# Optimization experiments

Hardware: AMD Instinct MI355X
Metric: run time of the kernel (lower is better)

Reference implementation:

```python
import jax, jax.numpy as jnp
import numpy as np
import math

TWO_PI = 2.0 * math.pi
LN_EPS = 1e-5


def _phase(pos_f, d):
    # periods[i, j] = i * d + j + 2 ; phi[s, i, j] = cos(2*pi*k_s / periods[i, j])
    i = jnp.arange(d, dtype=jnp.float32)
    periods = i[:, None] * d + i[None, :] + 2.0  # (d, d)
    return jnp.cos(TWO_PI * pos_f[:, None, None] / periods)  # (S, d, d)


def _layernorm(x, g, b):
    mu = jnp.mean(x, axis=-1, keepdims=True)
    var = jnp.mean(jnp.square(x - mu), axis=-1, keepdims=True)
    return (x - mu) * jax.lax.rsqrt(var + LN_EPS) * g + b


def _pos_nk(x, P, phi):
    # Nk[b, s, i] = sum_j P[i, j] * x[b, s, j] * phi[s, i, j]
    return jnp.einsum('bsj,ij,sij->bsi', x, P, phi)


def setup_inputs() -> dict:
    key = jax.random.key(0)
    ks = jax.random.split(key, 10)
    B, S, V, D = 4, 4096, 64, 128
    NTOK = 64  # 4^3 k-mer tokens
    u = lambda k, shp, a: jax.random.uniform(k, shp, jnp.float32, -a, a)
    return {
        'tokens': jax.random.randint(ks[0], (B, S), 0, NTOK, dtype=jnp.int32),
        'positions': jnp.arange(S, dtype=jnp.int32),
        'emb': jax.random.normal(ks[1], (NTOK, V), jnp.float32),
        'char_P': u(ks[2], (V, V), 0.1),
        'M1': u(ks[3], (D, V), 0.5),
        'P1': u(ks[4], (D, D), 0.1),
        'g1': jnp.ones((D,), jnp.float32),
        'b1': jnp.zeros((D,), jnp.float32),
        'R1': u(ks[5], (D, V), 0.1),
        'M2': u(ks[6], (D, D), 0.5),
        'P2': u(ks[7], (D, D), 0.1),
        'g2': jnp.ones((D,), jnp.float32),
        'b2': jnp.zeros((D,), jnp.float32),
    }


def reference(tokens, positions, emb, char_P, M1, P1, g1, b1, R1, M2, P2, g2, b2):
    pos_f = positions.astype(jnp.float32)
    V, D1, D2 = emb.shape[1], M1.shape[0], M2.shape[0]
    # char level (Layer 0): embedding + position-modulated mixing
    x = emb[tokens]                               # (B, S, V)
    h = _pos_nk(x, char_P, _phase(pos_f, V))      # (B, S, V)
    # Layer 1: separate residual (in_dim != out_dim -> linear proj)
    t1 = jnp.einsum('bsj,ij->bsi', h, M1)         # (B, S, D1)
    n1 = _pos_nk(_layernorm(t1, g1, b1), P1, _phase(pos_f, D1))
    h1 = n1 + jnp.einsum('bsj,ij->bsi', h, R1)
    # Layer 2: shared residual (residual = x @ M.T, pre-norm)
    t2 = jnp.einsum('bsj,ij->bsi', h1, M2)        # (B, S, D2)
    n2 = _pos_nk(_layernorm(t2, g2, b2), P2, _phase(pos_f, D2))
    return n2 + t2
```

## Files before the change

kernel.cpp:

```cpp
#include <hip/hip_runtime.h>

typedef unsigned short u16;
typedef unsigned int   u32;

#define BB 4
#define SS 4096
#define VV 64
#define DD 128

#define CPT_OFF 0
#define M1T_OFF 4096
#define R1T_OFF 12288
#define P1T_OFF 20480
#define M2T_OFF 36864
#define P2T_OFF 53248
#define EMB_OFF 69632
#define G1_OFF  73728
#define B1_OFF  73856
#define G2_OFF  73984
#define B2_OFF  74112
#define WS_F32_NEEDED 74240

__device__ __forceinline__ float bf2f(u16 u) {
    return __uint_as_float(((u32)u) << 16);
}
__device__ __forceinline__ float ldany(const void* p, int idx, bool f32) {
    return f32 ? ((const float*)p)[idx] : bf2f(((const u16*)p)[idx]);
}
__device__ __forceinline__ float phase_cos(float pos, float pf) {
    float x = pos * __builtin_amdgcn_rcpf(pf);
    float r = x - floorf(x);
    return __builtin_amdgcn_cosf(r);
}

__global__ void prep_ws(const void* __restrict__ cP,  const void* __restrict__ M1,
                        const void* __restrict__ R1,  const void* __restrict__ P1,
                        const void* __restrict__ M2,  const void* __restrict__ P2,
                        const void* __restrict__ emb, const void* __restrict__ g1,
                        const void* __restrict__ b1,  const void* __restrict__ g2,
                        const void* __restrict__ b2,  float* __restrict__ wsf)
{
    const bool f32 = (((const u32*)g1)[0] == 0x3F800000u);
    const int m = blockIdx.x;
    const int t = threadIdx.x;
    if (m == 6) {
        for (int idx = t; idx < 4608; idx += 256) {
            float v; int dst;
            if (idx < 4096) { v = ldany(emb, idx, f32); dst = EMB_OFF + idx; }
            else {
                int off = idx - 4096, which = off >> 7, e = off & 127;
                const void* p = (which == 0) ? g1 : (which == 1) ? b1
                              : (which == 2) ? g2 : b2;
                v = ldany(p, e, f32);
                dst = G1_OFF + which * 128 + e;
            }
            wsf[dst] = v;
        }
        return;
    }
    __shared__ float tile[64][65];
    const void* src; float* dst; int R, C;
    switch (m) {
        case 0:  src = cP; dst = wsf + CPT_OFF; R = 64;  C = 64;  break;
        case 1:  src = M1; dst = wsf + M1T_OFF; R = 128; C = 64;  break;
        case 2:  src = R1; dst = wsf + R1T_OFF; R = 128; C = 64;  break;
        case 3:  src = P1; dst = wsf + P1T_OFF; R = 128; C = 128; break;
        case 4:  src = M2; dst = wsf + M2T_OFF; R = 128; C = 128; break;
        default: src = P2; dst = wsf + P2T_OFF; R = 128; C = 128; break;
    }
    for (int ti0 = 0; ti0 < R; ti0 += 64) {
        for (int tj0 = 0; tj0 < C; tj0 += 64) {
            __syncthreads();
            #pragma unroll
            for (int k = 0; k < 16; ++k) {
                int idx = k * 256 + t;
                int i = idx >> 6, j = idx & 63;
                tile[i][j] = ldany(src, (ti0 + i) * C + (tj0 + j), f32);
            }
            __syncthreads();
            #pragma unroll
            for (int k = 0; k < 16; ++k) {
                int idx = k * 256 + t;
                int j = idx >> 6, i = idx & 63;
                int gj = tj0 + j, gi = ti0 + i;
                dst[((gj >> 2) * R + gi) * 4 + (gj & 3)] = tile[i][j];
            }
        }
    }
}

template<bool WS>
__global__ void __launch_bounds__(256, 4)
fused_hier(const int* __restrict__ tokens,
           const int* __restrict__ positions,
           const void* __restrict__ emb,
           const void* __restrict__ cP,
           const void* __restrict__ M1,
           const void* __restrict__ P1,
           const void* __restrict__ g1,
           const void* __restrict__ b1,
           const void* __restrict__ R1,
           const void* __restrict__ M2,
           const void* __restrict__ P2,
           const void* __restrict__ g2,
           const void* __restrict__ b2,
           const float* __restrict__ wsf,
           float* __restrict__ out)
{
    __shared__ float4 x4v[VV];
    __shared__ float4 h4v[VV];
    __shared__ float4 lnv[DD];
    __shared__ float4 h1v[DD];
    __shared__ float4 t2v[DD];
    __shared__ float4 partv[512];
    __shared__ float  t14[DD * BB];

    float* lnf  = (float*)lnv;
    float* h1f  = (float*)h1v;
    float* t2f  = (float*)t2v;
    float* part = (float*)partv;
    float* h4   = (float*)h4v;
    float* x4   = (float*)x4v;

    const int t = threadIdx.x;
    const int s = blockIdx.x;
    if (s >= SS) return;
    const bool f32 = WS ? true : (((const u32*)g1)[0] == 0x3F800000u);
    const float pos = (float)positions[s];
    const int i6 = t & 63,  q4 = t >> 6;
    const int i7 = t & 127, h2 = t >> 7;
    const int w  = t >> 6,  l  = t & 63;

    {
        int tok = tokens[q4 * SS + s];
        float v = WS ? wsf[EMB_OFF + tok * VV + i6] : ldany(emb, tok * VV + i6, f32);
        x4[i6 * 4 + q4] = v;
    }
    __syncthreads();

    {
        float a0 = 0.f, a1 = 0.f, a2 = 0.f, a3 = 0.f;
        const int jb = q4 * 16;
        float pf = (float)(i6 * VV + jb + 2);
        #pragma unroll
        for (int q = 0; q < 4; ++q) {
            const int jg = q4 * 4 + q;
            float4 w4;
            if (WS) w4 = *(const float4*)&wsf[CPT_OFF + (jg * VV + i6) * 4];
            #pragma unroll
            for (int k = 0; k < 4; ++k) {
                const int j = jb + q * 4 + k;
                float c  = phase_cos(pos, pf);
                float wt = (WS ? ((const float*)&w4)[k]
                               : ldany(cP, i6 * VV + j, f32)) * c;
                float4 xb = x4v[j];
                a0 = fmaf(wt, xb.x, a0); a1 = fmaf(wt, xb.y, a1);
                a2 = fmaf(wt, xb.z, a2); a3 = fmaf(wt, xb.w, a3);
                pf += 1.0f;
            }
        }
        partv[i6 * 4 + q4] = make_float4(a0, a1, a2, a3);
    }
    __syncthreads();

    {
        const int b = q4, i = i6;
        h4[i * 4 + b] = part[(i * 4 + 0) * 4 + b] + part[(i * 4 + 1) * 4 + b]
                      + part[(i * 4 + 2) * 4 + b] + part[(i * 4 + 3) * 4 + b];
    }
    __syncthreads();

    {
        float4 at = make_float4(0, 0, 0, 0), ar = make_float4(0, 0, 0, 0);
        #pragma unroll
        for (int q = 0; q < 8; ++q) {
            const int jg = h2 * 8 + q;
            float4 m4, r4;
            if (WS) {
                m4 = *(const float4*)&wsf[M1T_OFF + (jg * DD + i7) * 4];
                r4 = *(const float4*)&wsf[R1T_OFF + (jg * DD + i7) * 4];
            }
            #pragma unroll
            for (int k = 0; k < 4; ++k) {
                const int j = h2 * 32 + q * 4 + k;
                float mv = WS ? ((const float*)&m4)[k] : ldany(M1, i7 * VV + j, f32);
                float rv = WS ? ((const float*)&r4)[k] : ldany(R1, i7 * VV + j, f32);
                float4 hb = h4v[j];
                at.x = fmaf(mv, hb.x, at.x); at.y = fmaf(mv, hb.y, at.y);
                at.z = fmaf(mv, hb.z, at.z); at.w = fmaf(mv, hb.w, at.w);
                ar.x = fmaf(rv, hb.x, ar.x); ar.y = fmaf(rv, hb.y, ar.y);
                ar.z = fmaf(rv, hb.z, ar.z); ar.w = fmaf(rv, hb.w, ar.w);
            }
        }
        partv[i7 * 2 + h2]       = at;
        partv[256 + i7 * 2 + h2] = ar;
    }
    __syncthreads();

    {
        #pragma unroll
        for (int k = 0; k < 2; ++k) {
            const int b = h2 * 2 + k;
            t14[i7 * 4 + b] = part[(i7 * 2 + 0) * 4 + b] + part[(i7 * 2 + 1) * 4 + b];
            h1f[i7 * 4 + b] = part[1024 + (i7 * 2 + 0) * 4 + b]
                            + part[1024 + (i7 * 2 + 1) * 4 + b];
        }
    }
    __syncthreads();

    {
        float v0 = t14[l * 4 + w], v1 = t14[(l + 64) * 4 + w];
        float s1 = v0 + v1;
        #pragma unroll
        for (int m = 1; m < 64; m <<= 1) s1 += __shfl_xor(s1, m, 64);
        float mu = s1 * (1.0f / 128.0f);
        float d0 = v0 - mu, d1 = v1 - mu;
        float s2 = d0 * d0 + d1 * d1;
        #pragma unroll
        for (int m = 1; m < 64; m <<= 1) s2 += __shfl_xor(s2, m, 64);
        float rs = rsqrtf(s2 * (1.0f / 128.0f) + 1e-5f);
        float ga = WS ? wsf[G1_OFF + l]      : ldany(g1, l, f32);
        float gb = WS ? wsf[G1_OFF + l + 64] : ldany(g1, l + 64, f32);
        float ba = WS ? wsf[B1_OFF + l]      : ldany(b1, l, f32);
        float bb = WS ? wsf[B1_OFF + l + 64] : ldany(b1, l + 64, f32);
        lnf[l * 4 + w]        = d0 * rs * ga + ba;
        lnf[(l + 64) * 4 + w] = d1 * rs * gb + bb;
    }
    __syncthreads();

    {
        float4 acc = make_float4(0, 0, 0, 0);
        float pf = (float)(i7 * DD + h2 * 64 + 2);
        #pragma unroll
        for (int q = 0; q < 16; ++q) {
            const int jg = h2 * 16 + q;
            float4 w4;
            if (WS) w4 = *(const float4*)&wsf[P1T_OFF + (jg * DD + i7) * 4];
            #pragma unroll
            for (int k = 0; k < 4; ++k) {
                const int j = h2 * 64 + q * 4 + k;
                float c = phase_cos(pos, pf);
                float wt = (WS ? ((const float*)&w4)[k]
                               : ldany(P1, i7 * DD + j, f32)) * c;
                float4 lb = lnv[j];
                acc.x = fmaf(wt, lb.x, acc.x); acc.y = fmaf(wt, lb.y, acc.y);
                acc.z = fmaf(wt, lb.z, acc.z); acc.w = fmaf(wt, lb.w, acc.w);
                pf += 1.0f;
            }
        }
        partv[i7 * 2 + h2] = acc;
    }
    __syncthreads();

    {
        #pragma unroll
        for (int k = 0; k < 2; ++k) {
            const int b = h2 * 2 + k;
            h1f[i7 * 4 + b] += part[(i7 * 2 + 0) * 4 + b] + part[(i7 * 2 + 1) * 4 + b];
        }
    }
    __syncthreads();

    {
        float4 acc = make_float4(0, 0, 0, 0);
        #pragma unroll
        for (int q = 0; q < 16; ++q) {
            const int jg = h2 * 16 + q;
            float4 m4;
            if (WS) m4 = *(const float4*)&wsf[M2T_OFF + (jg * DD + i7) * 4];
            #pragma unroll
            for (int k = 0; k < 4; ++k) {
                const int j = h2 * 64 + q * 4 + k;
                float mv = WS ? ((const float*)&m4)[k] : ldany(M2, i7 * DD + j, f32);
                float4 hb = h1v[j];
                acc.x = fmaf(mv, hb.x, acc.x); acc.y = fmaf(mv, hb.y, acc.y);
                acc.z = fmaf(mv, hb.z, acc.z); acc.w = fmaf(mv, hb.w, acc.w);
            }
        }
        partv[i7 * 2 + h2] = acc;
    }
    __syncthreads();

    {
        #pragma unroll
        for (int k = 0; k < 2; ++k) {
            const int b = h2 * 2 + k;
            t2f[i7 * 4 + b] = part[(i7 * 2 + 0) * 4 + b] + part[(i7 * 2 + 1) * 4 + b];
        }
    }
    __syncthreads();

    {
        float v0 = t2f[l * 4 + w], v1 = t2f[(l + 64) * 4 + w];
        float s1 = v0 + v1;
        #pragma unroll
        for (int m = 1; m < 64; m <<= 1) s1 += __shfl_xor(s1, m, 64);
        float mu = s1 * (1.0f / 128.0f);
        float d0 = v0 - mu, d1 = v1 - mu;
        float s2 = d0 * d0 + d1 * d1;
        #pragma unroll
        for (int m = 1; m < 64; m <<= 1) s2 += __shfl_xor(s2, m, 64);
        float rs = rsqrtf(s2 * (1.0f / 128.0f) + 1e-5f);
        float ga = WS ? wsf[G2_OFF + l]      : ldany(g2, l, f32);
        float gb = WS ? wsf[G2_OFF + l + 64] : ldany(g2, l + 64, f32);
        float ba = WS ? wsf[B2_OFF + l]      : ldany(b2, l, f32);
        float bb = WS ? wsf[B2_OFF + l + 64] : ldany(b2, l + 64, f32);
        lnf[l * 4 + w]        = d0 * rs * ga + ba;
        lnf[(l + 64) * 4 + w] = d1 * rs * gb + bb;
    }
    __syncthreads();

    {
        float4 acc = make_float4(0, 0, 0, 0);
        float pf = (float)(i7 * DD + h2 * 64 + 2);
        #pragma unroll
        for (int q = 0; q < 16; ++q) {
            const int jg = h2 * 16 + q;
            float4 w4;
            if (WS) w4 = *(const float4*)&wsf[P2T_OFF + (jg * DD + i7) * 4];
            #pragma unroll
            for (int k = 0; k < 4; ++k) {
                const int j = h2 * 64 + q * 4 + k;
                float c = phase_cos(pos, pf);
                float wt = (WS ? ((const float*)&w4)[k]
                               : ldany(P2, i7 * DD + j, f32)) * c;
                float4 lb = lnv[j];
                acc.x = fmaf(wt, lb.x, acc.x); acc.y = fmaf(wt, lb.y, acc.y);
                acc.z = fmaf(wt, lb.z, acc.z); acc.w = fmaf(wt, lb.w, acc.w);
                pf += 1.0f;
            }
        }
        partv[i7 * 2 + h2] = acc;
    }
    __syncthreads();

    {
        #pragma unroll
        for (int k = 0; k < 2; ++k) {
            const int b = h2 * 2 + k;
            float v = part[(i7 * 2 + 0) * 4 + b] + part[(i7 * 2 + 1) * 4 + b]
                    + t2f[i7 * 4 + b];
            out[(b * SS + s) * DD + i7] = v;
        }
    }
}

extern "C" void kernel_launch(void* const* d_in, const int* in_sizes, int n_in,
                              void* d_out, int out_size, void* d_ws, size_t ws_size,
                              hipStream_t stream)
{
    const int* tokens    = (const int*)d_in[0];
    const int* positions = (const int*)d_in[1];
    const void* emb = d_in[2];
    const void* cP  = d_in[3];
    const void* M1  = d_in[4];
    const void* P1  = d_in[5];
    const void* g1  = d_in[6];
    const void* b1  = d_in[7];
    const void* R1  = d_in[8];
    const void* M2  = d_in[9];
    const void* P2  = d_in[10];
    const void* g2  = d_in[11];
    const void* b2  = d_in[12];
    float* out = (float*)d_out;
    float* wsf = (float*)d_ws;

    const bool tw = (ws_size >= (size_t)WS_F32_NEEDED * sizeof(float));
    if (tw) {
        prep_ws<<<7, 256, 0, stream>>>(cP, M1, R1, P1, M2, P2, emb, g1, b1, g2, b2, wsf);
        fused_hier<true><<<SS, 256, 0, stream>>>(tokens, positions, emb, cP, M1, P1,
                                                 g1, b1, R1, M2, P2, g2, b2, wsf, out);
    } else {
        fused_hier<false><<<SS, 256, 0, stream>>>(tokens, positions, emb, cP, M1, P1,
                                                  g1, b1, R1, M2, P2, g2, b2, wsf, out);
    }
}
```

Before: 168.8 us.

## Precompute bf16 phase-cosine table in workspace and reuse across layers

Adds a prep pass with one block per position that writes a bf16 table of the 128x128 phase cosines into workspace. The fused kernel loads these instead of evaluating rcp/floor/cos per element, and one table serves both the char layer (a 64x64 subset via period indexing) and both 128-wide layers. It also moves partial-sum buffers to a float4 batch-packed layout and simplifies reductions and output stores. The cost is about 128 MB of table writes and reads per call, plus bf16 rounding of the phase values.

```diff
diff --git a/kernel.cpp b/kernel.cpp
--- a/kernel.cpp
+++ b/kernel.cpp
@@ -19,7 +19,10 @@
 #define B1_OFF  73856
 #define G2_OFF  73984
 #define B2_OFF  74112
-#define WS_F32_NEEDED 74240
+#define WS_F32_WEIGHTS 74240
+#define PH_BYTE      ((size_t)WS_F32_WEIGHTS * 4)
+#define PH_ROW_BYTES 32768
+#define WS_BYTES_TABLE (PH_BYTE + (size_t)SS * (size_t)PH_ROW_BYTES)
 
 __device__ __forceinline__ float bf2f(u16 u) {
     return __uint_as_float(((u32)u) << 16);
@@ -31,6 +34,27 @@
     float x = pos * __builtin_amdgcn_rcpf(pf);
     float r = x - floorf(x);
     return __builtin_amdgcn_cosf(r);
+}
+__device__ __forceinline__ u32 f2bf(float f) {
+    u32 b = __float_as_uint(f);
+    b += 0x7FFFu + ((b >> 16) & 1u);
+    return b >> 16;
+}
+__device__ __forceinline__ float bfhalf(u32 word, int hi) {
+    return __uint_as_float(hi ? (word & 0xffff0000u) : (word << 16));
+}
+__device__ __forceinline__ u32 u4get(uint4 v, int i) {
+    return i == 0 ? v.x : i == 1 ? v.y : i == 2 ? v.z : v.w;
+}
+__device__ __forceinline__ float f4get(float4 v, int i) {
+    return i == 0 ? v.x : i == 1 ? v.y : i == 2 ? v.z : v.w;
+}
+__device__ __forceinline__ float4 f4sum(float4 a, float4 b) {
+    return make_float4(a.x + b.x, a.y + b.y, a.z + b.z, a.w + b.w);
+}
+__device__ __forceinline__ float4 fma4(float s, float4 v, float4 a) {
+    return make_float4(fmaf(s, v.x, a.x), fmaf(s, v.y, a.y),
+                       fmaf(s, v.z, a.z), fmaf(s, v.w, a.w));
 }
 
 __global__ void prep_ws(const void* __restrict__ cP,  const void* __restrict__ M1,
@@ -38,11 +62,32 @@
                         const void* __restrict__ M2,  const void* __restrict__ P2,
                         const void* __restrict__ emb, const void* __restrict__ g1,
                         const void* __restrict__ b1,  const void* __restrict__ g2,
-                        const void* __restrict__ b2,  float* __restrict__ wsf)
+                        const void* __restrict__ b2,  const int* __restrict__ positions,
+                        float* __restrict__ wsf)
 {
-    const bool f32 = (((const u32*)g1)[0] == 0x3F800000u);
     const int m = blockIdx.x;
     const int t = threadIdx.x;
+    if (m >= 7) {
+        const int s = m - 7;
+        const float pos = (float)positions[s];
+        const int i  = t & 127;
+        const int jh = t >> 7;
+        uint4* row = (uint4*)((char*)wsf + PH_BYTE + (size_t)s * PH_ROW_BYTES);
+        const float pb = (float)(i * DD + jh * 64 + 2);
+        #pragma unroll
+        for (int o = 0; o < 8; ++o) {
+            u32 pk[4];
+            #pragma unroll
+            for (int e = 0; e < 4; ++e) {
+                float c0 = phase_cos(pos, pb + (float)(o * 8 + 2 * e));
+                float c1 = phase_cos(pos, pb + (float)(o * 8 + 2 * e + 1));
+                pk[e] = f2bf(c0) | (f2bf(c1) << 16);
+            }
+            row[(jh * 8 + o) * 128 + i] = make_uint4(pk[0], pk[1], pk[2], pk[3]);
+        }
+        return;
+    }
+    const bool f32 = (((const u32*)g1)[0] == 0x3F800000u);
     if (m == 6) {
         for (int idx = t; idx < 4608; idx += 256) {
             float v; int dst;
@@ -89,7 +134,7 @@
     }
 }
 
-template<bool WS>
+template<int MODE>
 __global__ void __launch_bounds__(256, 4)
 fused_hier(const int* __restrict__ tokens,
            const int* __restrict__ positions,
@@ -107,20 +152,18 @@
            const float* __restrict__ wsf,
            float* __restrict__ out)
 {
+    constexpr bool WS = (MODE >= 1);
+    constexpr bool TB = (MODE == 2);
+
     __shared__ float4 x4v[VV];
     __shared__ float4 h4v[VV];
     __shared__ float4 lnv[DD];
     __shared__ float4 h1v[DD];
     __shared__ float4 t2v[DD];
+    __shared__ float4 t14v[DD];
     __shared__ float4 partv[512];
-    __shared__ float  t14[DD * BB];
-
-    float* lnf  = (float*)lnv;
-    float* h1f  = (float*)h1v;
-    float* t2f  = (float*)t2v;
-    float* part = (float*)partv;
-    float* h4   = (float*)h4v;
-    float* x4   = (float*)x4v;
+
+    float* lnf = (float*)lnv;
 
     const int t = threadIdx.x;
     const int s = blockIdx.x;
@@ -131,15 +174,30 @@
     const int i7 = t & 127, h2 = t >> 7;
     const int w  = t >> 6,  l  = t & 63;
 
-    {
-        int tok = tokens[q4 * SS + s];
-        float v = WS ? wsf[EMB_OFF + tok * VV + i6] : ldany(emb, tok * VV + i6, f32);
-        x4[i6 * 4 + q4] = v;
-    }
-    __syncthreads();
-
-    {
-        float a0 = 0.f, a1 = 0.f, a2 = 0.f, a3 = 0.f;
+    const uint4* phrow =
+        (const uint4*)((const char*)wsf + PH_BYTE + (size_t)s * PH_ROW_BYTES);
+
+    if (t < 64) {
+        int tk0 = tokens[0 * SS + s], tk1 = tokens[1 * SS + s];
+        int tk2 = tokens[2 * SS + s], tk3 = tokens[3 * SS + s];
+        float4 xb;
+        xb.x = WS ? wsf[EMB_OFF + tk0 * VV + i6] : ldany(emb, tk0 * VV + i6, f32);
+        xb.y = WS ? wsf[EMB_OFF + tk1 * VV + i6] : ldany(emb, tk1 * VV + i6, f32);
+        xb.z = WS ? wsf[EMB_OFF + tk2 * VV + i6] : ldany(emb, tk2 * VV + i6, f32);
+        xb.w = WS ? wsf[EMB_OFF + tk3 * VV + i6] : ldany(emb, tk3 * VV + i6, f32);
+        x4v[i6] = xb;
+    }
+    __syncthreads();
+
+    {
+        float4 a = make_float4(0, 0, 0, 0);
+        uint4 pcA, pcB;
+        if (TB) {
+            const int cb = (i6 & 1) * 8 + q4 * 2;
+            const int Ir = i6 >> 1;
+            pcA = phrow[(cb + 0) * 128 + Ir];
+            pcB = phrow[(cb + 1) * 128 + Ir];
+        }
         const int jb = q4 * 16;
         float pf = (float)(i6 * VV + jb + 2);
         #pragma unroll
@@ -149,26 +207,31 @@
             if (WS) w4 = *(const float4*)&wsf[CPT_OFF + (jg * VV + i6) * 4];
             #pragma unroll
             for (int k = 0; k < 4; ++k) {
-                const int j = jb + q * 4 + k;
-                float c  = phase_cos(pos, pf);
-                float wt = (WS ? ((const float*)&w4)[k]
-                               : ldany(cP, i6 * VV + j, f32)) * c;
-                float4 xb = x4v[j];
-                a0 = fmaf(wt, xb.x, a0); a1 = fmaf(wt, xb.y, a1);
-                a2 = fmaf(wt, xb.z, a2); a3 = fmaf(wt, xb.w, a3);
+                const int j  = jb + q * 4 + k;
+                const int kk = q * 4 + k;
+                float c;
+                if (TB) c = bfhalf(u4get(kk < 8 ? pcA : pcB, (kk >> 1) & 3), kk & 1);
+                else    c = phase_cos(pos, pf);
+                float wt = (WS ? f4get(w4, k) : ldany(cP, i6 * VV + j, f32)) * c;
+                a = fma4(wt, x4v[j], a);
                 pf += 1.0f;
             }
         }
-        partv[i6 * 4 + q4] = make_float4(a0, a1, a2, a3);
-    }
-    __syncthreads();
-
-    {
-        const int b = q4, i = i6;
-        h4[i * 4 + b] = part[(i * 4 + 0) * 4 + b] + part[(i * 4 + 1) * 4 + b]
-                      + part[(i * 4 + 2) * 4 + b] + part[(i * 4 + 3) * 4 + b];
-    }
-    __syncthreads();
+        partv[q4 * 64 + i6] = a;
+    }
+    __syncthreads();
+
+    if (t < 64) {
+        h4v[i6] = f4sum(f4sum(partv[i6], partv[64 + i6]),
+                        f4sum(partv[128 + i6], partv[192 + i6]));
+    }
+    __syncthreads();
+
+    uint4 ph[8];
+    if (TB) {
+        #pragma unroll
+        for (int o = 0; o < 8; ++o) ph[o] = phrow[(h2 * 8 + o) * 128 + i7];
+    }
 
     {
         float4 at = make_float4(0, 0, 0, 0), ar = make_float4(0, 0, 0, 0);
@@ -183,33 +246,26 @@
             #pragma unroll
             for (int k = 0; k < 4; ++k) {
                 const int j = h2 * 32 + q * 4 + k;
-                float mv = WS ? ((const float*)&m4)[k] : ldany(M1, i7 * VV + j, f32);
-                float rv = WS ? ((const float*)&r4)[k] : ldany(R1, i7 * VV + j, f32);
+                float mv = WS ? f4get(m4, k) : ldany(M1, i7 * VV + j, f32);
+                float rv = WS ? f4get(r4, k) : ldany(R1, i7 * VV + j, f32);
                 float4 hb = h4v[j];
-                at.x = fmaf(mv, hb.x, at.x); at.y = fmaf(mv, hb.y, at.y);
-                at.z = fmaf(mv, hb.z, at.z); at.w = fmaf(mv, hb.w, at.w);
-                ar.x = fmaf(rv, hb.x, ar.x); ar.y = fmaf(rv, hb.y, ar.y);
-                ar.z = fmaf(rv, hb.z, ar.z); ar.w = fmaf(rv, hb.w, ar.w);
-            }
-        }
-        partv[i7 * 2 + h2]       = at;
-        partv[256 + i7 * 2 + h2] = ar;
-    }
-    __syncthreads();
-
-    {
-        #pragma unroll
-        for (int k = 0; k < 2; ++k) {
-            const int b = h2 * 2 + k;
-            t14[i7 * 4 + b] = part[(i7 * 2 + 0) * 4 + b] + part[(i7 * 2 + 1) * 4 + b];
-            h1f[i7 * 4 + b] = part[1024 + (i7 * 2 + 0) * 4 + b]
-                            + part[1024 + (i7 * 2 + 1) * 4 + b];
-        }
-    }
-    __syncthreads();
-
-    {
-        float v0 = t14[l * 4 + w], v1 = t14[(l + 64) * 4 + w];
+                at = fma4(mv, hb, at);
+                ar = fma4(rv, hb, ar);
+            }
+        }
+        partv[h2 * 128 + i7]       = at;
+        partv[256 + h2 * 128 + i7] = ar;
+    }
+    __syncthreads();
+
+    if (t < 128) {
+        t14v[i7] = f4sum(partv[i7], partv[128 + i7]);
+        h1v[i7]  = f4sum(partv[256 + i7], partv[384 + i7]);
+    }
+    __syncthreads();
+
+    {
+        float v0 = f4get(t14v[l], w), v1 = f4get(t14v[l + 64], w);
         float s1 = v0 + v1;
         #pragma unroll
         for (int m = 1; m < 64; m <<= 1) s1 += __shfl_xor(s1, m, 64);
@@ -232,32 +288,30 @@
         float4 acc = make_float4(0, 0, 0, 0);
         float pf = (float)(i7 * DD + h2 * 64 + 2);
         #pragma unroll
-        for (int q = 0; q < 16; ++q) {
-            const int jg = h2 * 16 + q;
-            float4 w4;
-            if (WS) w4 = *(const float4*)&wsf[P1T_OFF + (jg * DD + i7) * 4];
-            #pragma unroll
-            for (int k = 0; k < 4; ++k) {
-                const int j = h2 * 64 + q * 4 + k;
-                float c = phase_cos(pos, pf);
-                float wt = (WS ? ((const float*)&w4)[k]
-                               : ldany(P1, i7 * DD + j, f32)) * c;
-                float4 lb = lnv[j];
-                acc.x = fmaf(wt, lb.x, acc.x); acc.y = fmaf(wt, lb.y, acc.y);
-                acc.z = fmaf(wt, lb.z, acc.z); acc.w = fmaf(wt, lb.w, acc.w);
+        for (int o = 0; o < 8; ++o) {
+            float4 wa, wb;
+            if (WS) {
+                wa = *(const float4*)&wsf[P1T_OFF + ((h2 * 16 + 2 * o    ) * DD + i7) * 4];
+                wb = *(const float4*)&wsf[P1T_OFF + ((h2 * 16 + 2 * o + 1) * DD + i7) * 4];
+            }
+            #pragma unroll
+            for (int e = 0; e < 8; ++e) {
+                const int j = h2 * 64 + o * 8 + e;
+                float c;
+                if (TB) c = bfhalf(u4get(ph[o], e >> 1), e & 1);
+                else    c = phase_cos(pos, pf);
+                float wv = WS ? (e < 4 ? f4get(wa, e) : f4get(wb, e - 4))
+                              : ldany(P1, i7 * DD + j, f32);
+                acc = fma4(wv * c, lnv[j], acc);
                 pf += 1.0f;
             }
         }
-        partv[i7 * 2 + h2] = acc;
-    }
-    __syncthreads();
-
-    {
-        #pragma unroll
-        for (int k = 0; k < 2; ++k) {
-            const int b = h2 * 2 + k;
-            h1f[i7 * 4 + b] += part[(i7 * 2 + 0) * 4 + b] + part[(i7 * 2 + 1) * 4 + b];
-        }
+        partv[h2 * 128 + i7] = acc;
+    }
+    __syncthreads();
+
+    if (t < 128) {
+        h1v[i7] = f4sum(h1v[i7], f4sum(partv[i7], partv[128 + i7]));
     }
     __syncthreads();
 
@@ -271,27 +325,21 @@
             #pragma unroll
             for (int k = 0; k < 4; ++k) {
                 const int j = h2 * 64 + q * 4 + k;
-                float mv = WS ? ((const float*)&m4)[k] : ldany(M2, i7 * DD + j, f32);
-                float4 hb = h1v[j];
-                acc.x = fmaf(mv, hb.x, acc.x); acc.y = fmaf(mv, hb.y, acc.y);
-                acc.z = fmaf(mv, hb.z, acc.z); acc.w = fmaf(mv, hb.w, acc.w);
-            }
-        }
-        partv[i7 * 2 + h2] = acc;
-    }
-    __syncthreads();
-
-    {
-        #pragma unroll
-        for (int k = 0; k < 2; ++k) {
-            const int b = h2 * 2 + k;
-            t2f[i7 * 4 + b] = part[(i7 * 2 + 0) * 4 + b] + part[(i7 * 2 + 1) * 4 + b];
-        }
-    }
-    __syncthreads();
-
-    {
-        float v0 = t2f[l * 4 + w], v1 = t2f[(l + 64) * 4 + w];
+                float mv = WS ? f4get(m4, k) : ldany(M2, i7 * DD + j, f32);
+                acc = fma4(mv, h1v[j], acc);
+            }
+        }
+        partv[h2 * 128 + i7] = acc;
+    }
+    __syncthreads();
+
+    if (t < 128) {
+        t2v[i7] = f4sum(partv[i7], partv[128 + i7]);
+    }
+    __syncthreads();
+
+    {
+        float v0 = f4get(t2v[l], w), v1 = f4get(t2v[l + 64], w);
         float s1 = v0 + v1;
         #pragma unroll
         for (int m = 1; m < 64; m <<= 1) s1 += __shfl_xor(s1, m, 64);
@@ -314,34 +362,35 @@
         float4 acc = make_float4(0, 0, 0, 0);
         float pf = (float)(i7 * DD + h2 * 64 + 2);
         #pragma unroll
-        for (int q = 0; q < 16; ++q) {
-            const int jg = h2 * 16 + q;
-            float4 w4;
-            if (WS) w4 = *(const float4*)&wsf[P2T_OFF + (jg * DD + i7) * 4];
-            #pragma unroll
-            for (int k = 0; k < 4; ++k) {
-                const int j = h2 * 64 + q * 4 + k;
-                float c = phase_cos(pos, pf);
-                float wt = (WS ? ((const float*)&w4)[k]
-                               : ldany(P2, i7 * DD + j, f32)) * c;
-                float4 lb = lnv[j];
-                acc.x = fmaf(wt, lb.x, acc.x); acc.y = fmaf(wt, lb.y, acc.y);
-                acc.z = fmaf(wt, lb.z, acc.z); acc.w = fmaf(wt, lb.w, acc.w);
+        for (int o = 0; o < 8; ++o) {
+            float4 wa, wb;
+            if (WS) {
+                wa = *(const float4*)&wsf[P2T_OFF + ((h2 * 16 + 2 * o    ) * DD + i7) * 4];
+                wb = *(const float4*)&wsf[P2T_OFF + ((h2 * 16 + 2 * o + 1) * DD + i7) * 4];
+            }
+            #pragma unroll
+            for (int e = 0; e < 8; ++e) {
+                const int j = h2 * 64 + o * 8 + e;
+                float c;
+                if (TB) c = bfhalf(u4get(ph[o], e >> 1), e & 1);
+                else    c = phase_cos(pos, pf);
+                float wv = WS ? (e < 4 ? f4get(wa, e) : f4get(wb, e - 4))
+                              : ldany(P2, i7 * DD + j, f32);
+                acc = fma4(wv * c, lnv[j], acc);
                 pf += 1.0f;
             }
         }
-        partv[i7 * 2 + h2] = acc;
-    }
-    __syncthreads();
-
-    {
-        #pragma unroll
-        for (int k = 0; k < 2; ++k) {
-            const int b = h2 * 2 + k;
-            float v = part[(i7 * 2 + 0) * 4 + b] + part[(i7 * 2 + 1) * 4 + b]
-                    + t2f[i7 * 4 + b];
-            out[(b * SS + s) * DD + i7] = v;
-        }
+        partv[h2 * 128 + i7] = acc;
+    }
+    __syncthreads();
+
+    if (t < 128) {
+        float4 n2 = f4sum(partv[i7], partv[128 + i7]);
+        float4 o4 = f4sum(n2, t2v[i7]);
+        out[(0 * SS + s) * DD + i7] = o4.x;
+        out[(1 * SS + s) * DD + i7] = o4.y;
+        out[(2 * SS + s) * DD + i7] = o4.z;
+        out[(3 * SS + s) * DD + i7] = o4.w;
     }
 }
 
@@ -365,13 +414,20 @@
     float* out = (float*)d_out;
     float* wsf = (float*)d_ws;
 
-    const bool tw = (ws_size >= (size_t)WS_F32_NEEDED * sizeof(float));
-    if (tw) {
-        prep_ws<<<7, 256, 0, stream>>>(cP, M1, R1, P1, M2, P2, emb, g1, b1, g2, b2, wsf);
-        fused_hier<true><<<SS, 256, 0, stream>>>(tokens, positions, emb, cP, M1, P1,
-                                                 g1, b1, R1, M2, P2, g2, b2, wsf, out);
+    const bool tab = (ws_size >= WS_BYTES_TABLE);
+    const bool tw  = (ws_size >= (size_t)WS_F32_WEIGHTS * sizeof(float));
+    if (tab) {
+        prep_ws<<<7 + SS, 256, 0, stream>>>(cP, M1, R1, P1, M2, P2, emb,
+                                            g1, b1, g2, b2, positions, wsf);
+        fused_hier<2><<<SS, 256, 0, stream>>>(tokens, positions, emb, cP, M1, P1,
+                                              g1, b1, R1, M2, P2, g2, b2, wsf, out);
+    } else if (tw) {
+        prep_ws<<<7, 256, 0, stream>>>(cP, M1, R1, P1, M2, P2, emb,
+                                       g1, b1, g2, b2, positions, wsf);
+        fused_hier<1><<<SS, 256, 0, stream>>>(tokens, positions, emb, cP, M1, P1,
+                                              g1, b1, R1, M2, P2, g2, b2, wsf, out);
     } else {
-        fused_hier<false><<<SS, 256, 0, stream>>>(tokens, positions, emb, cP, M1, P1,
-                                                  g1, b1, R1, M2, P2, g2, b2, wsf, out);
-    }
-}
+        fused_hier<0><<<SS, 256, 0, stream>>>(tokens, positions, emb, cP, M1, P1,
+                                              g1, b1, R1, M2, P2, g2, b2, wsf, out);
+    }
+}
```

After: 228.0 us. +35.1%, slower.
